# Kernel optimization log

Hardware: AMD Instinct MI355X
Metric: run time of the kernel (lower is better)

## Reference

```python
import jax, jax.numpy as jnp
import numpy as np

CTX2 = [-2, 1]
CTX3 = [-3, 3]
CTX4 = [-7, 2]


def _tdnn(x, kernel, bias, ctx_list):
    # x: [B,T,I], kernel: [O,I,K]; replaces the per-timestep index_select+conv1d loop
    T = x.shape[1]
    start = max(0, -ctx_list[0])
    end = T - ctx_list[-1] if ctx_list[-1] > 0 else T
    idx = jnp.arange(start, end)[:, None] + jnp.asarray(ctx_list)[None, :]  # [Tout,K]
    xg = x[:, idx, :]  # [B,Tout,K,I] gathered context frames
    return jnp.einsum('btki,oik->bto', xg, kernel) + bias


def _res(x, w1, b1, w2, b2, rbias):
    # ResBlock (dropout = identity in eval)
    h = jax.nn.relu(x @ w1.T + b1)
    h = h @ w2.T + b2
    return jax.nn.relu(h + x + rbias)


def _forward(x, fc1_w, fc1_b,
             res1_w1, res1_b1, res1_w2, res1_b2, res1_bias,
             tdnn2_k, tdnn2_b,
             res2_w1, res2_b1, res2_w2, res2_b2, res2_bias,
             tdnn3_k, tdnn3_b,
             res3_w1, res3_b1, res3_w2, res3_b2, res3_bias,
             tdnn4_k, tdnn4_b,
             res4_w1, res4_b1, res4_w2, res4_b2, res4_bias,
             bnf_w, bnf_b, ws1, ws2, bnw_w, bnw_b):
    h = jax.nn.relu(x @ fc1_w.T + fc1_b)
    h = _res(h, res1_w1, res1_b1, res1_w2, res1_b2, res1_bias)
    h = jax.nn.relu(_tdnn(h, tdnn2_k, tdnn2_b, CTX2))
    h = _res(h, res2_w1, res2_b1, res2_w2, res2_b2, res2_bias)
    h = jax.nn.relu(_tdnn(h, tdnn3_k, tdnn3_b, CTX3))
    h = _res(h, res3_w1, res3_b1, res3_w2, res3_b2, res3_bias)
    h = jax.nn.relu(_tdnn(h, tdnn4_k, tdnn4_b, CTX4))
    h = _res(h, res4_w1, res4_b1, res4_w2, res4_b2, res4_bias)
    h = h @ bnf_w.T + bnf_b  # [B,T',128]
    A = jax.nn.softmax(jnp.tanh(h @ ws1.T) @ ws2.T, axis=1)  # softmax over time, [B,T',heads]
    At = jnp.swapaxes(A, 1, 2)  # [B,heads,T']
    pooled = jnp.einsum('bht,btd->bhd', At, h)  # [B,heads,128]
    out = jax.nn.relu(pooled.reshape(pooled.shape[0], -1) @ bnw_w.T + bnw_b)
    return out, At


def setup_inputs() -> dict:
    B, T, D, H = 64, 800, 500, 512
    key = jax.random.key(0)
    ks = iter(jax.random.split(key, 40))
    stdv_lin = lambda fan: 1.0 / np.sqrt(fan)

    def lin(fan_in, fan_out):
        s = stdv_lin(fan_in)
        return (jax.random.uniform(next(ks), (fan_out, fan_in), jnp.float32, -s, s),
                jax.random.uniform(next(ks), (fan_out,), jnp.float32, -s, s))

    inp = {}
    inp['x'] = jax.random.normal(next(ks), (B, T, D), jnp.float32)
    inp['fc1_w'], inp['fc1_b'] = lin(D, H)
    for i in (1, 2, 3, 4):
        inp[f'res{i}_w1'], inp[f'res{i}_b1'] = lin(H, H)
        inp[f'res{i}_w2'], inp[f'res{i}_b2'] = lin(H, H)
        inp[f'res{i}_bias'] = jnp.ones((H,), jnp.float32)
    s = 1.0 / np.sqrt(H)
    for i in (2, 3, 4):
        inp[f'tdnn{i}_k'] = jax.random.normal(next(ks), (H, H, 2), jnp.float32) * s
        inp[f'tdnn{i}_b'] = jax.random.normal(next(ks), (H,), jnp.float32) * s
    inp['bnf_w'], inp['bnf_b'] = lin(H, 128)
    inp['ws1'] = jax.random.uniform(next(ks), (128, 128), jnp.float32, -0.1, 0.1)
    inp['ws2'] = jax.random.uniform(next(ks), (5, 128), jnp.float32, -0.1, 0.1)
    inp['bnw_w'], inp['bnw_b'] = lin(640, 128)
    return inp


def reference(x, fc1_w, fc1_b,
              res1_w1, res1_b1, res1_w2, res1_b2, res1_bias,
              res2_w1, res2_b1, res2_w2, res2_b2, res2_bias,
              res3_w1, res3_b1, res3_w2, res3_b2, res3_bias,
              res4_w1, res4_b1, res4_w2, res4_b2, res4_bias,
              tdnn2_k, tdnn2_b, tdnn3_k, tdnn3_b, tdnn4_k, tdnn4_b,
              bnf_w, bnf_b, ws1, ws2, bnw_w, bnw_b):
    return _forward(x, fc1_w, fc1_b,
                    res1_w1, res1_b1, res1_w2, res1_b2, res1_bias,
                    tdnn2_k, tdnn2_b,
                    res2_w1, res2_b1, res2_w2, res2_b2, res2_bias,
                    tdnn3_k, tdnn3_b,
                    res3_w1, res3_b1, res3_w2, res3_b2, res3_bias,
                    tdnn4_k, tdnn4_b,
                    res4_w1, res4_b1, res4_w2, res4_b2, res4_bias,
                    bnf_w, bnf_b, ws1, ws2, bnw_w, bnw_b)
```

## Files before the change

kernel.cpp:

```cpp
#include <hip/hip_runtime.h>
#include <hip/hip_bf16.h>

typedef unsigned short ushort_t;
typedef __attribute__((ext_vector_type(8))) short short8;
typedef __attribute__((ext_vector_type(4))) float f32x4;

__device__ __forceinline__ float bf2f(unsigned short u) {
  union { unsigned int i; float f; } v; v.i = ((unsigned int)u) << 16; return v.f;
}
__device__ __forceinline__ unsigned short f2bf(float f) {
  union { float f; unsigned int i; } v; v.f = f;
  unsigned int u = v.i;
  unsigned int r = (u + 0x7fffu + ((u >> 16) & 1u)) >> 16;
  return (unsigned short)r;
}

__device__ __forceinline__ void gload16(const void* g, void* l) {
  __builtin_amdgcn_global_load_lds(
      (const __attribute__((address_space(1))) void*)g,
      (__attribute__((address_space(3))) void*)l, 16, 0, 0);
}

template<int KTOT, int ACT, bool RES>
__global__ __launch_bounds__(256, 4) void gemm_kernel(
    const ushort_t* __restrict__ A, const ushort_t* __restrict__ W,
    const float* __restrict__ bias,
    const ushort_t* __restrict__ resin, const float* __restrict__ resbias,
    ushort_t* __restrict__ out,
    int M, int Ntot, int T_in, int T_out, int sh1, int ncb)
{
  constexpr int AROW = (KTOT == 1024) ? 512 : KTOT;
  __shared__ ushort_t As[128 * 64];
  __shared__ ushort_t Ws[128 * 64];

  const int tid = threadIdx.x;
  const int lane = tid & 63;
  const int w = tid >> 6;
  const int wm = w >> 1, wn = w & 1;

  const int nblocks = (int)gridDim.x;
  const int xcd = blockIdx.x & 7, kk = blockIdx.x >> 3;
  const int q = nblocks >> 3, rr = nblocks & 7;
  const int L = xcd * q + (xcd < rr ? xcd : rr) + kk;
  int rowblk, colblk;
  if (ncb == 4) { rowblk = L >> 2; colblk = L & 3; }
  else          { rowblk = L;      colblk = 0; }
  const int blockN = colblk * 128;
  const int blockRow = rowblk * 128;

  const int b0 = blockRow / T_out;
  const int t0 = blockRow - b0 * T_out;

  f32x4 acc[4][4];
#pragma unroll
  for (int i = 0; i < 4; ++i)
#pragma unroll
    for (int j = 0; j < 4; ++j) acc[i][j] = f32x4{0.f, 0.f, 0.f, 0.f};

  const int mloc = tid >> 3;
  const int csw = (((tid & 7) ^ ((tid >> 3) & 7))) * 8;

  for (int k0 = 0; k0 < KTOT; k0 += 64) {
    const int kcol = k0 & (AROW - 1);
    const int rowoff = (KTOT == 1024 && k0 >= 512) ? sh1 : 0;
#pragma unroll
    for (int j = 0; j < 4; ++j) {
      int m = j * 32 + mloc;
      int r = blockRow + m;
      int t = t0 + m;
      int bb = b0;
      if (t >= T_out) { ++bb; t -= T_out; }
      long grow = (r < M) ? ((long)bb * T_in + t + rowoff)
                          : ((long)b0 * T_in + t0 + rowoff);
      gload16(A + grow * AROW + kcol + csw, (char*)As + (j * 4096 + tid * 16));
    }
#pragma unroll
    for (int j = 0; j < 4; ++j) {
      int n = blockN + j * 32 + mloc;
      gload16(W + (long)n * KTOT + k0 + csw, (char*)Ws + (j * 4096 + tid * 16));
    }
    __syncthreads();
#pragma unroll
    for (int ks = 0; ks < 64; ks += 32) {
      short8 af[4], bf[4];
      const int hi = lane >> 4;
      const int rlo = lane & 15;
#pragma unroll
      for (int f = 0; f < 4; ++f) {
        int row = wm * 64 + f * 16 + rlo;
        int chunk = (ks >> 3) + hi;
        af[f] = *reinterpret_cast<const short8*>(
            (const char*)As + row * 128 + ((chunk ^ (row & 7)) << 4));
      }
#pragma unroll
      for (int f = 0; f < 4; ++f) {
        int row = wn * 64 + f * 16 + rlo;
        int chunk = (ks >> 3) + hi;
        bf[f] = *reinterpret_cast<const short8*>(
            (const char*)Ws + row * 128 + ((chunk ^ (row & 7)) << 4));
      }
#pragma unroll
      for (int fm = 0; fm < 4; ++fm)
#pragma unroll
        for (int fn = 0; fn < 4; ++fn)
          acc[fm][fn] = __builtin_amdgcn_mfma_f32_16x16x32_bf16(af[fm], bf[fn], acc[fm][fn], 0, 0, 0);
    }
    __syncthreads();
  }

  const int colb = lane & 15;
  const int rowb = (lane >> 4) * 4;
  float bv[4];
#pragma unroll
  for (int fn = 0; fn < 4; ++fn) {
    int col = blockN + wn * 64 + fn * 16 + colb;
    float b = bias ? bias[col] : 0.f;
    if (RES) b += resbias[col];
    bv[fn] = b;
  }
#pragma unroll
  for (int fm = 0; fm < 4; ++fm) {
#pragma unroll
    for (int reg = 0; reg < 4; ++reg) {
      int r = blockRow + wm * 64 + fm * 16 + rowb + reg;
      if (r < M) {
#pragma unroll
        for (int fn = 0; fn < 4; ++fn) {
          int col = blockN + wn * 64 + fn * 16 + colb;
          float v = acc[fm][fn][reg] + bv[fn];
          if (RES) v += bf2f(resin[(long)r * 512 + col]);
          if (ACT == 1) v = fmaxf(v, 0.f);
          else if (ACT == 2) v = tanhf(v);
          out[(long)r * Ntot + col] = f2bf(v);
        }
      }
    }
  }
}

__global__ __launch_bounds__(256) void pad512_f32_kernel(
    const float* __restrict__ in, ushort_t* __restrict__ out, long total, int Kin)
{
  long g = ((long)blockIdx.x * 256 + threadIdx.x) * 4;
  if (g >= total) return;
  int r = (int)(g >> 9), c = (int)(g & 511);
  ushort_t o0 = 0, o1 = 0, o2 = 0, o3 = 0;
  if (c < Kin) {
    float4 v = *(const float4*)(in + (long)r * Kin + c);
    o0 = f2bf(v.x); o1 = f2bf(v.y); o2 = f2bf(v.z); o3 = f2bf(v.w);
  }
  unsigned long long pk = (unsigned long long)o0 | ((unsigned long long)o1 << 16) |
                          ((unsigned long long)o2 << 32) | ((unsigned long long)o3 << 48);
  *(unsigned long long*)(out + g) = pk;
}

__global__ __launch_bounds__(256) void repack_tdnn_f32_kernel(
    const float* __restrict__ in, ushort_t* __restrict__ out)
{
  int g = blockIdx.x * 256 + threadIdx.x;
  int o = g >> 10, rem = g & 1023;
  int s = rem >> 9, i = rem & 511;
  out[g] = f2bf(in[(o << 10) + (i << 1) + s]);
}

__global__ __launch_bounds__(256) void cvt_kernel(
    const float* __restrict__ in, ushort_t* __restrict__ out, int n)
{
  int g = (blockIdx.x * 256 + threadIdx.x) * 4;
  if (g >= n) return;
  float4 v = *(const float4*)(in + g);
  unsigned long long pk = (unsigned long long)f2bf(v.x) | ((unsigned long long)f2bf(v.y) << 16) |
                          ((unsigned long long)f2bf(v.z) << 32) | ((unsigned long long)f2bf(v.w) << 48);
  *(unsigned long long*)(out + g) = pk;
}

__global__ __launch_bounds__(320) void attn_kernel(
    const ushort_t* __restrict__ s1, const float* __restrict__ ws2,
    float* __restrict__ At_out, int T)
{
  __shared__ float w2s[640];
  __shared__ float sc[800 * 5];
  int b = blockIdx.x, tid = threadIdx.x;
  for (int i = tid; i < 640; i += 320) w2s[i] = ws2[i];
  __syncthreads();
  for (int t = tid; t < T; t += 320) {
    const ushort_t* row = s1 + ((long)b * T + t) * 128;
    float a0 = 0, a1 = 0, a2 = 0, a3 = 0, a4 = 0;
    for (int c = 0; c < 128; c += 8) {
      short8 v = *reinterpret_cast<const short8*>(row + c);
#pragma unroll
      for (int j = 0; j < 8; ++j) {
        float xv = bf2f((unsigned short)v[j]);
        a0 += xv * w2s[0 * 128 + c + j];
        a1 += xv * w2s[1 * 128 + c + j];
        a2 += xv * w2s[2 * 128 + c + j];
        a3 += xv * w2s[3 * 128 + c + j];
        a4 += xv * w2s[4 * 128 + c + j];
      }
    }
    sc[t * 5 + 0] = a0; sc[t * 5 + 1] = a1; sc[t * 5 + 2] = a2;
    sc[t * 5 + 3] = a3; sc[t * 5 + 4] = a4;
  }
  __syncthreads();
  int h = tid >> 6, ln = tid & 63;
  float m = -1e30f;
  for (int t = ln; t < T; t += 64) m = fmaxf(m, sc[t * 5 + h]);
#pragma unroll
  for (int off = 32; off > 0; off >>= 1) m = fmaxf(m, __shfl_xor(m, off));
  float s = 0.f;
  for (int t = ln; t < T; t += 64) s += expf(sc[t * 5 + h] - m);
#pragma unroll
  for (int off = 32; off > 0; off >>= 1) s += __shfl_xor(s, off);
  float inv = 1.f / s;
  long base = ((long)b * 5 + h) * T;
  for (int t = ln; t < T; t += 64)
    At_out[base + t] = expf(sc[t * 5 + h] - m) * inv;
}

__global__ __launch_bounds__(640) void pool_kernel(
    const float* __restrict__ At_f, const ushort_t* __restrict__ hb,
    float* __restrict__ pooled, int T)
{
  int b = blockIdx.x, tid = threadIdx.x;
  int h = tid >> 7, d = tid & 127;
  const float* at = At_f + ((long)b * 5 + h) * T;
  const ushort_t* hr = hb + (long)b * T * 128 + d;
  float acc = 0.f;
  int t = 0;
  for (; t + 4 <= T; t += 4) {
    acc += at[t]     * bf2f(hr[(long)(t) * 128]);
    acc += at[t + 1] * bf2f(hr[(long)(t + 1) * 128]);
    acc += at[t + 2] * bf2f(hr[(long)(t + 2) * 128]);
    acc += at[t + 3] * bf2f(hr[(long)(t + 3) * 128]);
  }
  for (; t < T; ++t) acc += at[t] * bf2f(hr[(long)t * 128]);
  pooled[b * 640 + tid] = acc;
}

__global__ __launch_bounds__(128) void head_kernel(
    const float* __restrict__ pooled, const float* __restrict__ w,
    const float* __restrict__ bias, float* __restrict__ out)
{
  int b = blockIdx.x, o = threadIdx.x;
  const float* wr = w + o * 640;
  const float* p = pooled + b * 640;
  float acc = bias[o];
  for (int i = 0; i < 640; i += 4)
    acc += p[i] * wr[i] + p[i + 1] * wr[i + 1] +
           p[i + 2] * wr[i + 2] + p[i + 3] * wr[i + 3];
  out[b * 128 + o] = fmaxf(acc, 0.f);
}

extern "C" void kernel_launch(void* const* d_in, const int* in_sizes, int n_in,
                              void* d_out, int out_size, void* d_ws, size_t ws_size,
                              hipStream_t stream)
{
  (void)in_sizes; (void)n_in; (void)out_size; (void)ws_size;
  const float* x     = (const float*)d_in[0];
  const float* fc1_w = (const float*)d_in[1];
  const float* fc1_b = (const float*)d_in[2];
  const float *rw1[4], *rb1[4], *rw2[4], *rb2[4], *rbias[4];
  for (int i = 0; i < 4; ++i) {
    rw1[i]   = (const float*)d_in[3 + 5 * i + 0];
    rb1[i]   = (const float*)d_in[3 + 5 * i + 1];
    rw2[i]   = (const float*)d_in[3 + 5 * i + 2];
    rb2[i]   = (const float*)d_in[3 + 5 * i + 3];
    rbias[i] = (const float*)d_in[3 + 5 * i + 4];
  }
  const float *tk[3], *tb[3];
  for (int i = 0; i < 3; ++i) {
    tk[i] = (const float*)d_in[23 + 2 * i];
    tb[i] = (const float*)d_in[24 + 2 * i];
  }
  const float* bnf_w = (const float*)d_in[29];
  const float* bnf_b = (const float*)d_in[30];
  const float* ws1   = (const float*)d_in[31];
  const float* ws2   = (const float*)d_in[32];
  const float* bnw_w = (const float*)d_in[33];
  const float* bnw_b = (const float*)d_in[34];

  char* ws = (char*)d_ws;
  const size_t SZBUF = (size_t)51200 * 512 * 2;
  ushort_t* bufA = (ushort_t*)(ws);
  ushort_t* bufB = (ushort_t*)(ws + SZBUF);
  ushort_t* bufC = (ushort_t*)(ws + 2 * SZBUF);
  ushort_t* wfc1 = (ushort_t*)(ws + 3 * SZBUF);
  ushort_t* w2[3];
  w2[0] = wfc1 + 512 * 512;
  w2[1] = w2[0] + 512 * 1024;
  w2[2] = w2[1] + 512 * 1024;
  ushort_t* rwc[8];
  rwc[0] = w2[2] + 512 * 1024;
  for (int i = 1; i < 8; ++i) rwc[i] = rwc[i - 1] + 512 * 512;
  ushort_t* bnfwc = rwc[7] + 512 * 512;
  ushort_t* ws1c  = bnfwc + 128 * 512;
  float* pooled   = (float*)(ws1c + 128 * 128);

  float* out_f = (float*)d_out;
  float* At_f  = out_f + 8192;

  dim3 blk(256);
  {
    long totalx = (long)51200 * 512;
    pad512_f32_kernel<<<dim3((unsigned)((totalx / 4 + 255) / 256)), blk, 0, stream>>>(x, bufA, totalx, 500);
    long totalw = (long)512 * 512;
    pad512_f32_kernel<<<dim3((unsigned)((totalw / 4 + 255) / 256)), blk, 0, stream>>>(fc1_w, wfc1, totalw, 500);
    for (int i = 0; i < 3; ++i)
      repack_tdnn_f32_kernel<<<dim3(2048), blk, 0, stream>>>(tk[i], w2[i]);
    for (int i = 0; i < 4; ++i) {
      cvt_kernel<<<dim3(256), blk, 0, stream>>>(rw1[i], rwc[2 * i], 512 * 512);
      cvt_kernel<<<dim3(256), blk, 0, stream>>>(rw2[i], rwc[2 * i + 1], 512 * 512);
    }
    cvt_kernel<<<dim3(64), blk, 0, stream>>>(bnf_w, bnfwc, 128 * 512);
    cvt_kernel<<<dim3(16), blk, 0, stream>>>(ws1, ws1c, 128 * 128);
  }
  gemm_kernel<512, 1, false><<<dim3(1600), blk, 0, stream>>>(bufA, wfc1, fc1_b, nullptr, nullptr, bufB, 51200, 512, 51200, 51200, 0, 4);
  gemm_kernel<512, 1, false><<<dim3(1600), blk, 0, stream>>>(bufB, rwc[0], rb1[0], nullptr, nullptr, bufC, 51200, 512, 51200, 51200, 0, 4);
  gemm_kernel<512, 1, true ><<<dim3(1600), blk, 0, stream>>>(bufC, rwc[1], rb2[0], bufB, rbias[0], bufA, 51200, 512, 51200, 51200, 0, 4);
  gemm_kernel<1024, 1, false><<<dim3(1596), blk, 0, stream>>>(bufA, w2[0], tb[0], nullptr, nullptr, bufB, 51008, 512, 800, 797, 3, 4);
  gemm_kernel<512, 1, false><<<dim3(1596), blk, 0, stream>>>(bufB, rwc[2], rb1[1], nullptr, nullptr, bufC, 51008, 512, 51008, 51008, 0, 4);
  gemm_kernel<512, 1, true ><<<dim3(1596), blk, 0, stream>>>(bufC, rwc[3], rb2[1], bufB, rbias[1], bufA, 51008, 512, 51008, 51008, 0, 4);
  gemm_kernel<1024, 1, false><<<dim3(1584), blk, 0, stream>>>(bufA, w2[1], tb[1], nullptr, nullptr, bufB, 50624, 512, 797, 791, 6, 4);
  gemm_kernel<512, 1, false><<<dim3(1584), blk, 0, stream>>>(bufB, rwc[4], rb1[2], nullptr, nullptr, bufC, 50624, 512, 50624, 50624, 0, 4);
  gemm_kernel<512, 1, true ><<<dim3(1584), blk, 0, stream>>>(bufC, rwc[5], rb2[2], bufB, rbias[2], bufA, 50624, 512, 50624, 50624, 0, 4);
  gemm_kernel<1024, 1, false><<<dim3(1564), blk, 0, stream>>>(bufA, w2[2], tb[2], nullptr, nullptr, bufB, 50048, 512, 791, 782, 9, 4);
  gemm_kernel<512, 1, false><<<dim3(1564), blk, 0, stream>>>(bufB, rwc[6], rb1[3], nullptr, nullptr, bufC, 50048, 512, 50048, 50048, 0, 4);
  gemm_kernel<512, 1, true ><<<dim3(1564), blk, 0, stream>>>(bufC, rwc[7], rb2[3], bufB, rbias[3], bufA, 50048, 512, 50048, 50048, 0, 4);
  gemm_kernel<512, 0, false><<<dim3(391), blk, 0, stream>>>(bufA, bnfwc, bnf_b, nullptr, nullptr, bufB, 50048, 128, 50048, 50048, 0, 1);
  gemm_kernel<128, 2, false><<<dim3(391), blk, 0, stream>>>(bufB, ws1c, nullptr, nullptr, nullptr, bufC, 50048, 128, 50048, 50048, 0, 1);
  attn_kernel<<<dim3(64), dim3(320), 0, stream>>>(bufC, ws2, At_f, 782);
  pool_kernel<<<dim3(64), dim3(640), 0, stream>>>(At_f, bufB, pooled, 782);
  head_kernel<<<dim3(64), dim3(128), 0, stream>>>(pooled, bnw_w, bnw_b, out_f);
}
```

Measured before the change: 689.5 us.

## Replace main GEMMs with 256x256-tile 8-wave kernel with interleaved prefetch pipeline

Adds a new GEMM kernel using 256x256 output tiles, 512 threads (8 waves), and 128 KB of LDS double buffering. Global-to-LDS loads for the next k-tiles are interleaved with four MFMA phases separated by barriers, and s_setprio raises priority during the MFMA phases. Block indices are remapped across XCDs. It is used for the twelve 512-wide layers, aiming for more operand reuse per loaded byte and better overlap of loads with compute. The trade-off is fewer blocks (about 400 on the device), heavier register use, and a larger LDS footprint per block.

```diff
diff --git a/kernel.cpp b/kernel.cpp
--- a/kernel.cpp
+++ b/kernel.cpp
@@ -19,6 +19,188 @@
   __builtin_amdgcn_global_load_lds(
       (const __attribute__((address_space(1))) void*)g,
       (__attribute__((address_space(3))) void*)l, 16, 0, 0);
+}
+
+#define FULL_BAR() do { asm volatile("" ::: "memory"); \
+  __builtin_amdgcn_s_barrier(); asm volatile("" ::: "memory"); } while (0)
+
+template<int KTOT, bool RES>
+__global__ __launch_bounds__(512, 2) void gemm256p8(
+    const ushort_t* __restrict__ A, const ushort_t* __restrict__ W,
+    const float* __restrict__ bias,
+    const ushort_t* __restrict__ resin, const float* __restrict__ resbias,
+    ushort_t* __restrict__ out,
+    int M, int T_in, int T_out, int sh1)
+{
+  constexpr int NT = KTOT / 64;
+  __shared__ char lds[131072];
+
+  const int tid = threadIdx.x;
+  const int lane = tid & 63;
+  const int w = tid >> 6;
+  const int wm = w >> 2, wn = w & 3;
+
+  const int nblocks = (int)gridDim.x;
+  const int xcd = blockIdx.x & 7, kk = blockIdx.x >> 3;
+  const int q = nblocks >> 3, rr = nblocks & 7;
+  const int L = xcd * q + (xcd < rr ? xcd : rr) + kk;
+  const int blockRow = (L >> 1) * 256;
+  const int blockN   = (L & 1) * 256;
+
+  const int b0 = blockRow / T_out;
+  const int t0 = blockRow - b0 * T_out;
+
+  int lrow[2], chunkv[2];
+  long agb[2][2], wgb[2][2];
+#pragma unroll
+  for (int i = 0; i < 2; ++i) {
+    lrow[i] = (w * 2 + i) * 8 + (lane >> 3);
+    chunkv[i] = ((lane & 7) ^ (lrow[i] & 7)) * 8;
+  }
+#pragma unroll
+  for (int h = 0; h < 2; ++h)
+#pragma unroll
+    for (int i = 0; i < 2; ++i) {
+      int m = h * 128 + lrow[i];
+      int r = blockRow + m;
+      int t = t0 + m;
+      int bb = b0;
+      if (t >= T_out) { ++bb; t -= T_out; }
+      long grow = (r < M) ? ((long)bb * T_in + t) : ((long)b0 * T_in + t0);
+      agb[h][i] = grow * 512 + chunkv[i];
+      wgb[h][i] = (long)(blockN + m) * KTOT + chunkv[i];
+    }
+  const int ldst0 = w * 2048 + lane * 16;
+
+  auto stageA = [&](int d, int h, int kt) {
+    const int kcol = (kt * 64) & 511;
+    const int roff = (KTOT == 1024 && kt >= 8) ? sh1 * 512 : 0;
+    char* base = lds + d * 32768 + h * 16384 + ldst0;
+#pragma unroll
+    for (int i = 0; i < 2; ++i)
+      gload16(A + agb[h][i] + kcol + roff, base + i * 1024);
+  };
+  auto stageB = [&](int d, int h, int kt) {
+    char* base = lds + 65536 + d * 32768 + h * 16384 + ldst0;
+#pragma unroll
+    for (int i = 0; i < 2; ++i)
+      gload16(W + wgb[h][i] + kt * 64, base + i * 1024);
+  };
+
+  const int rlo = lane & 15, hi4 = lane >> 4;
+  auto ldA = [&](int d, int f, int ks) -> short8 {
+    int lr = f * 16 + rlo;
+    return *(const short8*)(lds + d * 32768 + wm * 16384 + lr * 128 +
+                            (((ks * 4 + hi4) ^ (lr & 7)) << 4));
+  };
+  auto ldB = [&](int d, int f2, int ks) -> short8 {
+    int lr = (wn & 1) * 64 + f2 * 16 + rlo;
+    return *(const short8*)(lds + 65536 + d * 32768 + (wn >> 1) * 16384 + lr * 128 +
+                            (((ks * 4 + hi4) ^ (lr & 7)) << 4));
+  };
+
+  f32x4 acc[8][4];
+#pragma unroll
+  for (int i = 0; i < 8; ++i)
+#pragma unroll
+    for (int j = 0; j < 4; ++j) acc[i][j] = f32x4{0.f, 0.f, 0.f, 0.f};
+  short8 afr[4][2], b0r[2][2], b1r[2][2];
+
+  stageB(0, 0, 0); stageA(0, 0, 0); stageA(0, 1, 0); stageB(0, 1, 0);
+  stageB(1, 0, 1); stageA(1, 0, 1);
+  asm volatile("s_waitcnt vmcnt(4)" ::: "memory");
+  FULL_BAR();
+
+  auto ktile = [&](int kt, int d) {
+#pragma unroll
+    for (int f = 0; f < 4; ++f) { afr[f][0] = ldA(d, f, 0); afr[f][1] = ldA(d, f, 1); }
+#pragma unroll
+    for (int f2 = 0; f2 < 2; ++f2) { b0r[f2][0] = ldB(d, f2, 0); b0r[f2][1] = ldB(d, f2, 1); }
+    if (kt + 1 < NT) stageA(d ^ 1, 1, kt + 1);
+    FULL_BAR();
+    __builtin_amdgcn_s_setprio(1);
+#pragma unroll
+    for (int fm = 0; fm < 4; ++fm)
+#pragma unroll
+      for (int fn = 0; fn < 2; ++fn)
+#pragma unroll
+        for (int ks = 0; ks < 2; ++ks)
+          acc[fm][fn] = __builtin_amdgcn_mfma_f32_16x16x32_bf16(afr[fm][ks], b0r[fn][ks], acc[fm][fn], 0, 0, 0);
+    __builtin_amdgcn_s_setprio(0);
+    FULL_BAR();
+#pragma unroll
+    for (int f2 = 0; f2 < 2; ++f2) { b1r[f2][0] = ldB(d, f2 + 2, 0); b1r[f2][1] = ldB(d, f2 + 2, 1); }
+    if (kt + 1 < NT) stageB(d ^ 1, 1, kt + 1);
+    FULL_BAR();
+    __builtin_amdgcn_s_setprio(1);
+#pragma unroll
+    for (int fm = 0; fm < 4; ++fm)
+#pragma unroll
+      for (int fn = 0; fn < 2; ++fn)
+#pragma unroll
+        for (int ks = 0; ks < 2; ++ks)
+          acc[fm][fn + 2] = __builtin_amdgcn_mfma_f32_16x16x32_bf16(afr[fm][ks], b1r[fn][ks], acc[fm][fn + 2], 0, 0, 0);
+    __builtin_amdgcn_s_setprio(0);
+    FULL_BAR();
+#pragma unroll
+    for (int f = 0; f < 4; ++f) { afr[f][0] = ldA(d, f + 4, 0); afr[f][1] = ldA(d, f + 4, 1); }
+    if (kt + 2 < NT) stageB(d, 0, kt + 2);
+    FULL_BAR();
+    __builtin_amdgcn_s_setprio(1);
+#pragma unroll
+    for (int fm = 0; fm < 4; ++fm)
+#pragma unroll
+      for (int fn = 0; fn < 2; ++fn)
+#pragma unroll
+        for (int ks = 0; ks < 2; ++ks)
+          acc[fm + 4][fn] = __builtin_amdgcn_mfma_f32_16x16x32_bf16(afr[fm][ks], b0r[fn][ks], acc[fm + 4][fn], 0, 0, 0);
+    __builtin_amdgcn_s_setprio(0);
+    FULL_BAR();
+    if (kt + 2 < NT) stageA(d, 0, kt + 2);
+    FULL_BAR();
+    __builtin_amdgcn_s_setprio(1);
+#pragma unroll
+    for (int fm = 0; fm < 4; ++fm)
+#pragma unroll
+      for (int fn = 0; fn < 2; ++fn)
+#pragma unroll
+        for (int ks = 0; ks < 2; ++ks)
+          acc[fm + 4][fn + 2] = __builtin_amdgcn_mfma_f32_16x16x32_bf16(afr[fm][ks], b1r[fn][ks], acc[fm + 4][fn + 2], 0, 0, 0);
+    __builtin_amdgcn_s_setprio(0);
+    if (kt + 2 < NT) asm volatile("s_waitcnt vmcnt(4)" ::: "memory");
+    else             asm volatile("s_waitcnt vmcnt(0)" ::: "memory");
+    FULL_BAR();
+  };
+
+  for (int kt2 = 0; kt2 < NT; kt2 += 2) { ktile(kt2, 0); ktile(kt2 + 1, 1); }
+
+  const int colb = rlo;
+  const int rowb = hi4 * 4;
+  float bv[4];
+#pragma unroll
+  for (int fn = 0; fn < 4; ++fn) {
+    int col = blockN + wn * 64 + fn * 16 + colb;
+    float b = bias[col];
+    if (RES) b += resbias[col];
+    bv[fn] = b;
+  }
+#pragma unroll
+  for (int fm = 0; fm < 8; ++fm) {
+#pragma unroll
+    for (int reg = 0; reg < 4; ++reg) {
+      int r = blockRow + wm * 128 + fm * 16 + rowb + reg;
+      if (r < M) {
+#pragma unroll
+        for (int fn = 0; fn < 4; ++fn) {
+          int col = blockN + wn * 64 + fn * 16 + colb;
+          float v = acc[fm][fn][reg] + bv[fn];
+          if (RES) v += bf2f(resin[(long)r * 512 + col]);
+          v = fmaxf(v, 0.f);
+          out[(long)r * 512 + col] = f2bf(v);
+        }
+      }
+    }
+  }
 }
 
 template<int KTOT, int ACT, bool RES>
@@ -300,6 +482,7 @@
   float* At_f  = out_f + 8192;
 
   dim3 blk(256);
+  dim3 blk512(512);
   {
     long totalx = (long)51200 * 512;
     pad512_f32_kernel<<<dim3((unsigned)((totalx / 4 + 255) / 256)), blk, 0, stream>>>(x, bufA, totalx, 500);
@@ -314,18 +497,18 @@
     cvt_kernel<<<dim3(64), blk, 0, stream>>>(bnf_w, bnfwc, 128 * 512);
     cvt_kernel<<<dim3(16), blk, 0, stream>>>(ws1, ws1c, 128 * 128);
   }
-  gemm_kernel<512, 1, false><<<dim3(1600), blk, 0, stream>>>(bufA, wfc1, fc1_b, nullptr, nullptr, bufB, 51200, 512, 51200, 51200, 0, 4);
-  gemm_kernel<512, 1, false><<<dim3(1600), blk, 0, stream>>>(bufB, rwc[0], rb1[0], nullptr, nullptr, bufC, 51200, 512, 51200, 51200, 0, 4);
-  gemm_kernel<512, 1, true ><<<dim3(1600), blk, 0, stream>>>(bufC, rwc[1], rb2[0], bufB, rbias[0], bufA, 51200, 512, 51200, 51200, 0, 4);
-  gemm_kernel<1024, 1, false><<<dim3(1596), blk, 0, stream>>>(bufA, w2[0], tb[0], nullptr, nullptr, bufB, 51008, 512, 800, 797, 3, 4);
-  gemm_kernel<512, 1, false><<<dim3(1596), blk, 0, stream>>>(bufB, rwc[2], rb1[1], nullptr, nullptr, bufC, 51008, 512, 51008, 51008, 0, 4);
-  gemm_kernel<512, 1, true ><<<dim3(1596), blk, 0, stream>>>(bufC, rwc[3], rb2[1], bufB, rbias[1], bufA, 51008, 512, 51008, 51008, 0, 4);
-  gemm_kernel<1024, 1, false><<<dim3(1584), blk, 0, stream>>>(bufA, w2[1], tb[1], nullptr, nullptr, bufB, 50624, 512, 797, 791, 6, 4);
-  gemm_kernel<512, 1, false><<<dim3(1584), blk, 0, stream>>>(bufB, rwc[4], rb1[2], nullptr, nullptr, bufC, 50624, 512, 50624, 50624, 0, 4);
-  gemm_kernel<512, 1, true ><<<dim3(1584), blk, 0, stream>>>(bufC, rwc[5], rb2[2], bufB, rbias[2], bufA, 50624, 512, 50624, 50624, 0, 4);
-  gemm_kernel<1024, 1, false><<<dim3(1564), blk, 0, stream>>>(bufA, w2[2], tb[2], nullptr, nullptr, bufB, 50048, 512, 791, 782, 9, 4);
-  gemm_kernel<512, 1, false><<<dim3(1564), blk, 0, stream>>>(bufB, rwc[6], rb1[3], nullptr, nullptr, bufC, 50048, 512, 50048, 50048, 0, 4);
-  gemm_kernel<512, 1, true ><<<dim3(1564), blk, 0, stream>>>(bufC, rwc[7], rb2[3], bufB, rbias[3], bufA, 50048, 512, 50048, 50048, 0, 4);
+  gemm256p8<512, false><<<dim3(400), blk512, 0, stream>>>(bufA, wfc1, fc1_b, nullptr, nullptr, bufB, 51200, 51200, 51200, 0);
+  gemm256p8<512, false><<<dim3(400), blk512, 0, stream>>>(bufB, rwc[0], rb1[0], nullptr, nullptr, bufC, 51200, 51200, 51200, 0);
+  gemm256p8<512, true ><<<dim3(400), blk512, 0, stream>>>(bufC, rwc[1], rb2[0], bufB, rbias[0], bufA, 51200, 51200, 51200, 0);
+  gemm256p8<1024, false><<<dim3(400), blk512, 0, stream>>>(bufA, w2[0], tb[0], nullptr, nullptr, bufB, 51008, 800, 797, 3);
+  gemm256p8<512, false><<<dim3(400), blk512, 0, stream>>>(bufB, rwc[2], rb1[1], nullptr, nullptr, bufC, 51008, 51008, 51008, 0);
+  gemm256p8<512, true ><<<dim3(400), blk512, 0, stream>>>(bufC, rwc[3], rb2[1], bufB, rbias[1], bufA, 51008, 51008, 51008, 0);
+  gemm256p8<1024, false><<<dim3(396), blk512, 0, stream>>>(bufA, w2[1], tb[1], nullptr, nullptr, bufB, 50624, 797, 791, 6);
+  gemm256p8<512, false><<<dim3(396), blk512, 0, stream>>>(bufB, rwc[4], rb1[2], nullptr, nullptr, bufC, 50624, 50624, 50624, 0);
+  gemm256p8<512, true ><<<dim3(396), blk512, 0, stream>>>(bufC, rwc[5], rb2[2], bufB, rbias[2], bufA, 50624, 50624, 50624, 0);
+  gemm256p8<1024, false><<<dim3(392), blk512, 0, stream>>>(bufA, w2[2], tb[2], nullptr, nullptr, bufB, 50048, 791, 782, 9);
+  gemm256p8<512, false><<<dim3(392), blk512, 0, stream>>>(bufB, rwc[6], rb1[3], nullptr, nullptr, bufC, 50048, 50048, 50048, 0);
+  gemm256p8<512, true ><<<dim3(392), blk512, 0, stream>>>(bufC, rwc[7], rb2[3], bufB, rbias[3], bufA, 50048, 50048, 50048, 0);
   gemm_kernel<512, 0, false><<<dim3(391), blk, 0, stream>>>(bufA, bnfwc, bnf_b, nullptr, nullptr, bufB, 50048, 128, 50048, 50048, 0, 1);
   gemm_kernel<128, 2, false><<<dim3(391), blk, 0, stream>>>(bufB, ws1c, nullptr, nullptr, nullptr, bufC, 50048, 128, 50048, 50048, 0, 1);
   attn_kernel<<<dim3(64), dim3(320), 0, stream>>>(bufC, ws2, At_f, 782);
```

Result: slower. 831.2 us (+20.6%).
